# Optimization experiments

Measured on AMD Instinct MI355X. Metric: run time of the kernel, lower is better.

Reference implementation:

```python
import jax, jax.numpy as jnp
from jax import lax
import numpy as np

B, CIN, COUT, H, W = 32, 64, 64, 128, 128
KH = KW = 1
STRIDE = (1, 1)
PADDING = ((0, 0), (0, 0))


def setup_inputs() -> dict:
    key = jax.random.key(0)
    k1, k2, k3, k4 = jax.random.split(key, 4)
    x_quant = jax.random.randint(k1, (B, CIN, H, W), 0, 256, dtype=jnp.int32)  # uint8 values
    weight_int8 = jax.random.randint(k2, (COUT, CIN, KH, KW), -127, 128, dtype=jnp.int32)
    weight_scale = jax.random.uniform(k3, (COUT, 1, 1, 1), dtype=jnp.float32, minval=0.001, maxval=0.02)
    weight_zero_point = jnp.zeros((COUT, 1, 1, 1), dtype=jnp.int32)
    bias_fp32 = jax.random.normal(k4, (COUT,), dtype=jnp.float32) * 0.1
    return {
        "x_quant": x_quant,
        "input_scale": jnp.float32(0.02),
        "input_zero_point": jnp.int32(128),
        "weight_int8": weight_int8,
        "weight_scale": weight_scale,
        "weight_zero_point": weight_zero_point,
        "bias_fp32": bias_fp32,
        "output_scale": jnp.float32(0.05),
        "output_zero_point": jnp.int32(128),
    }


def reference(x_quant, input_scale, input_zero_point, weight_int8, weight_scale,
              weight_zero_point, bias_fp32, output_scale, output_zero_point):
    # dequant (zero-point subtract) in fp32
    x = x_quant.astype(jnp.float32) - input_zero_point.astype(jnp.float32)          # [B,Cin,H,W]
    w = weight_int8.astype(jnp.float32) - weight_zero_point.astype(jnp.float32)     # [O,I,kh,kw]
    conv = lax.conv_general_dilated(
        x, w, window_strides=STRIDE, padding=PADDING,
        dimension_numbers=("NCHW", "OIHW", "NCHW"))                                 # [B,O,H',W']
    # requantize: per-out-channel scale + bias, round, clamp to uint8 range
    requant_scale = (input_scale * weight_scale / output_scale).reshape(1, COUT, 1, 1)
    bias_term = (bias_fp32 / output_scale).reshape(1, COUT, 1, 1)
    final_float = conv * requant_scale + bias_term
    requant = jnp.round(final_float) + output_zero_point.astype(jnp.float32)
    out_q = jnp.clip(requant, 0.0, 255.0).astype(jnp.uint8)
    return out_q
```

## Files before the change

### kernel.cpp

```cpp
#include <hip/hip_runtime.h>

#define CIN   64
#define COUT  64
#define HW    16384
#define NPIX  (32 * HW)
#define HALF  (NPIX / 2)

__global__ void prep_kernel(const int* __restrict__ w,
                            const float* __restrict__ wscale,
                            const int* __restrict__ wzp,
                            const float* __restrict__ bias,
                            const float* __restrict__ is_p,
                            const int* __restrict__ izp_p,
                            const float* __restrict__ os_p,
                            const int* __restrict__ ozp_p,
                            int* __restrict__ wp,
                            float4* __restrict__ params) {
    int o = threadIdx.x;
    if (o >= COUT) return;
    int zp = wzp[o];
    int sum = 0;
    #pragma unroll
    for (int k = 0; k < 16; ++k) {
        int c0 = w[o * CIN + 4 * k + 0] - zp;
        int c1 = w[o * CIN + 4 * k + 1] - zp;
        int c2 = w[o * CIN + 4 * k + 2] - zp;
        int c3 = w[o * CIN + 4 * k + 3] - zp;
        sum += c0 + c1 + c2 + c3;
        wp[o * 16 + k] = (c0 & 0xff) | ((c1 & 0xff) << 8) |
                         ((c2 & 0xff) << 16) | ((c3 & 0xff) << 24);
    }
    float4 pr;
    pr.x = is_p[0] * wscale[o] / os_p[0];
    pr.y = bias[o] / os_p[0] + (float)ozp_p[0];
    pr.z = 0.0f;
    pr.w = __int_as_float((128 - izp_p[0]) * sum);
    params[o] = pr;
}

__device__ __forceinline__ int pack4(int v0, int v1, int v2, int v3) {
    return (v0 | (v1 << 8) | (v2 << 16) | (v3 << 24)) ^ 0x80808080;
}

__global__ __launch_bounds__(128) void conv_kernel(
    const int* __restrict__ x,
    const int* __restrict__ wp_g,
    const float4* __restrict__ params_g,
    int* __restrict__ out) {

    const int tid = threadIdx.x;
    const int t0  = blockIdx.x * 128 + tid;

    #pragma unroll
    for (int half = 0; half < 2; ++half) {
        int t = t0 + half * HALF;
        int b = t >> 14;
        int p = t & (HW - 1);

        const int* xb = x + b * (CIN * HW) + p;

        int pk[16];
        #pragma unroll
        for (int cg = 0; cg < 16; ++cg) {
            int v0 = xb[(4 * cg + 0) * HW];
            int v1 = xb[(4 * cg + 1) * HW];
            int v2 = xb[(4 * cg + 2) * HW];
            int v3 = xb[(4 * cg + 3) * HW];
            pk[cg] = pack4(v0, v1, v2, v3);
        }

        int* ob = out + b * (COUT * HW) + p;

        #pragma unroll 8
        for (int o = 0; o < COUT; ++o) {
            const int4* wv = (const int4*)(wp_g + o * 16);
            int4 w0 = wv[0], w1 = wv[1], w2 = wv[2], w3 = wv[3];
            float4 pr = params_g[o];
            int acc = __float_as_int(pr.w);

            acc = __builtin_amdgcn_sdot4(pk[0],  w0.x, acc, false);
            acc = __builtin_amdgcn_sdot4(pk[1],  w0.y, acc, false);
            acc = __builtin_amdgcn_sdot4(pk[2],  w0.z, acc, false);
            acc = __builtin_amdgcn_sdot4(pk[3],  w0.w, acc, false);
            acc = __builtin_amdgcn_sdot4(pk[4],  w1.x, acc, false);
            acc = __builtin_amdgcn_sdot4(pk[5],  w1.y, acc, false);
            acc = __builtin_amdgcn_sdot4(pk[6],  w1.z, acc, false);
            acc = __builtin_amdgcn_sdot4(pk[7],  w1.w, acc, false);
            acc = __builtin_amdgcn_sdot4(pk[8],  w2.x, acc, false);
            acc = __builtin_amdgcn_sdot4(pk[9],  w2.y, acc, false);
            acc = __builtin_amdgcn_sdot4(pk[10], w2.z, acc, false);
            acc = __builtin_amdgcn_sdot4(pk[11], w2.w, acc, false);
            acc = __builtin_amdgcn_sdot4(pk[12], w3.x, acc, false);
            acc = __builtin_amdgcn_sdot4(pk[13], w3.y, acc, false);
            acc = __builtin_amdgcn_sdot4(pk[14], w3.z, acc, false);
            acc = __builtin_amdgcn_sdot4(pk[15], w3.w, acc, false);

            float f = fmaf((float)acc, pr.x, pr.y);
            f = rintf(f);
            f = fminf(fmaxf(f, 0.0f), 255.0f);
            __builtin_nontemporal_store((int)f, ob + o * HW);
        }
    }
}

extern "C" void kernel_launch(void* const* d_in, const int* in_sizes, int n_in,
                              void* d_out, int out_size, void* d_ws, size_t ws_size,
                              hipStream_t stream) {
    const int*   x      = (const int*)d_in[0];
    const float* is_p   = (const float*)d_in[1];
    const int*   izp_p  = (const int*)d_in[2];
    const int*   w      = (const int*)d_in[3];
    const float* wscale = (const float*)d_in[4];
    const int*   wzp    = (const int*)d_in[5];
    const float* bias   = (const float*)d_in[6];
    const float* os_p   = (const float*)d_in[7];
    const int*   ozp_p  = (const int*)d_in[8];

    int* out = (int*)d_out;

    int*    wp     = (int*)d_ws;
    float4* params = (float4*)((char*)d_ws + 4096);

    prep_kernel<<<1, 64, 0, stream>>>(w, wscale, wzp, bias, is_p, izp_p, os_p,
                                      ozp_p, wp, params);

    conv_kernel<<<2048, 128, 0, stream>>>(x, wp, params, out);
}
```

Before: 258.1 us.

## Prefetch second pixel's input channels while computing first pixel's outputs

Each thread handles two pixels. The loads for the second pixel's 64 input channels are now issued in chunks of 16, interleaved with the output computation and stores for the first pixel, so memory latency overlaps with sdot4 work. The aim is to hide load latency in a memory-bound kernel, at the cost of more live registers (16 raw values plus two packed arrays), which could lower occupancy.

```diff
diff --git a/kernel.cpp b/kernel.cpp
--- a/kernel.cpp
+++ b/kernel.cpp
@@ -42,65 +42,84 @@
     return (v0 | (v1 << 8) | (v2 << 16) | (v3 << 24)) ^ 0x80808080;
 }
 
+__device__ __forceinline__ void out_chunk(int o0,
+                                          const int* __restrict__ wp_g,
+                                          const float4* __restrict__ params_g,
+                                          const int pk[16],
+                                          int* __restrict__ ob) {
+    #pragma unroll
+    for (int i = 0; i < 16; ++i) {
+        int o = o0 + i;
+        const int4* wv = (const int4*)(wp_g + o * 16);
+        int4 w0 = wv[0], w1 = wv[1], w2 = wv[2], w3 = wv[3];
+        float4 pr = params_g[o];
+        int acc = __float_as_int(pr.w);
+
+        acc = __builtin_amdgcn_sdot4(pk[0],  w0.x, acc, false);
+        acc = __builtin_amdgcn_sdot4(pk[1],  w0.y, acc, false);
+        acc = __builtin_amdgcn_sdot4(pk[2],  w0.z, acc, false);
+        acc = __builtin_amdgcn_sdot4(pk[3],  w0.w, acc, false);
+        acc = __builtin_amdgcn_sdot4(pk[4],  w1.x, acc, false);
+        acc = __builtin_amdgcn_sdot4(pk[5],  w1.y, acc, false);
+        acc = __builtin_amdgcn_sdot4(pk[6],  w1.z, acc, false);
+        acc = __builtin_amdgcn_sdot4(pk[7],  w1.w, acc, false);
+        acc = __builtin_amdgcn_sdot4(pk[8],  w2.x, acc, false);
+        acc = __builtin_amdgcn_sdot4(pk[9],  w2.y, acc, false);
+        acc = __builtin_amdgcn_sdot4(pk[10], w2.z, acc, false);
+        acc = __builtin_amdgcn_sdot4(pk[11], w2.w, acc, false);
+        acc = __builtin_amdgcn_sdot4(pk[12], w3.x, acc, false);
+        acc = __builtin_amdgcn_sdot4(pk[13], w3.y, acc, false);
+        acc = __builtin_amdgcn_sdot4(pk[14], w3.z, acc, false);
+        acc = __builtin_amdgcn_sdot4(pk[15], w3.w, acc, false);
+
+        float f = fmaf((float)acc, pr.x, pr.y);
+        f = rintf(f);
+        f = fminf(fmaxf(f, 0.0f), 255.0f);
+        __builtin_nontemporal_store((int)f, ob + o * HW);
+    }
+}
+
 __global__ __launch_bounds__(128) void conv_kernel(
     const int* __restrict__ x,
     const int* __restrict__ wp_g,
     const float4* __restrict__ params_g,
     int* __restrict__ out) {
 
-    const int tid = threadIdx.x;
-    const int t0  = blockIdx.x * 128 + tid;
+    const int t = blockIdx.x * 128 + threadIdx.x;
+    const int bA = t >> 14, pA = t & (HW - 1);
+    const int tB = t + HALF;
+    const int bB = tB >> 14, pB = tB & (HW - 1);
+
+    const int* xA = x + bA * (CIN * HW) + pA;
+    const int* xB = x + bB * (CIN * HW) + pB;
+    int* obA = out + bA * (COUT * HW) + pA;
+    int* obB = out + bB * (COUT * HW) + pB;
+
+    int pkA[16];
+    #pragma unroll
+    for (int cg = 0; cg < 16; ++cg)
+        pkA[cg] = pack4(xA[(4 * cg + 0) * HW], xA[(4 * cg + 1) * HW],
+                        xA[(4 * cg + 2) * HW], xA[(4 * cg + 3) * HW]);
+
+    int pkB[16];
+    #pragma unroll
+    for (int c = 0; c < 4; ++c) {
+        int raw[16];
+        #pragma unroll
+        for (int j = 0; j < 16; ++j)
+            raw[j] = xB[(16 * c + j) * HW];
+
+        out_chunk(16 * c, wp_g, params_g, pkA, obA);
+
+        #pragma unroll
+        for (int g = 0; g < 4; ++g)
+            pkB[4 * c + g] = pack4(raw[4 * g + 0], raw[4 * g + 1],
+                                   raw[4 * g + 2], raw[4 * g + 3]);
+    }
 
     #pragma unroll
-    for (int half = 0; half < 2; ++half) {
-        int t = t0 + half * HALF;
-        int b = t >> 14;
-        int p = t & (HW - 1);
-
-        const int* xb = x + b * (CIN * HW) + p;
-
-        int pk[16];
-        #pragma unroll
-        for (int cg = 0; cg < 16; ++cg) {
-            int v0 = xb[(4 * cg + 0) * HW];
-            int v1 = xb[(4 * cg + 1) * HW];
-            int v2 = xb[(4 * cg + 2) * HW];
-            int v3 = xb[(4 * cg + 3) * HW];
-            pk[cg] = pack4(v0, v1, v2, v3);
-        }
-
-        int* ob = out + b * (COUT * HW) + p;
-
-        #pragma unroll 8
-        for (int o = 0; o < COUT; ++o) {
-            const int4* wv = (const int4*)(wp_g + o * 16);
-            int4 w0 = wv[0], w1 = wv[1], w2 = wv[2], w3 = wv[3];
-            float4 pr = params_g[o];
-            int acc = __float_as_int(pr.w);
-
-            acc = __builtin_amdgcn_sdot4(pk[0],  w0.x, acc, false);
-            acc = __builtin_amdgcn_sdot4(pk[1],  w0.y, acc, false);
-            acc = __builtin_amdgcn_sdot4(pk[2],  w0.z, acc, false);
-            acc = __builtin_amdgcn_sdot4(pk[3],  w0.w, acc, false);
-            acc = __builtin_amdgcn_sdot4(pk[4],  w1.x, acc, false);
-            acc = __builtin_amdgcn_sdot4(pk[5],  w1.y, acc, false);
-            acc = __builtin_amdgcn_sdot4(pk[6],  w1.z, acc, false);
-            acc = __builtin_amdgcn_sdot4(pk[7],  w1.w, acc, false);
-            acc = __builtin_amdgcn_sdot4(pk[8],  w2.x, acc, false);
-            acc = __builtin_amdgcn_sdot4(pk[9],  w2.y, acc, false);
-            acc = __builtin_amdgcn_sdot4(pk[10], w2.z, acc, false);
-            acc = __builtin_amdgcn_sdot4(pk[11], w2.w, acc, false);
-            acc = __builtin_amdgcn_sdot4(pk[12], w3.x, acc, false);
-            acc = __builtin_amdgcn_sdot4(pk[13], w3.y, acc, false);
-            acc = __builtin_amdgcn_sdot4(pk[14], w3.z, acc, false);
-            acc = __builtin_amdgcn_sdot4(pk[15], w3.w, acc, false);
-
-            float f = fmaf((float)acc, pr.x, pr.y);
-            f = rintf(f);
-            f = fminf(fmaxf(f, 0.0f), 255.0f);
-            __builtin_nontemporal_store((int)f, ob + o * HW);
-        }
-    }
+    for (int c = 0; c < 4; ++c)
+        out_chunk(16 * c, wp_g, params_g, pkB, obB);
 }
 
 extern "C" void kernel_launch(void* const* d_in, const int* in_sizes, int n_in,
```

After: 283.6 us. 9.9% more time.

## Map lanes to output channels with readlane broadcast and LDS-transposed stores

Applied to the files above, without the earlier changes.

Each lane now owns one output channel and keeps its packed weights in registers. Per pixel, the packed activations are broadcast across the wave with readlane, and the results are transposed through shared memory so the global stores stay coalesced. This removes the repeated per-output-channel weight loads from global memory and the second pass over pixels per thread. In exchange it adds readlane instructions (scalar-register traffic) and an LDS round trip, and it serialises pixels within a wave. Correctness depends on the readlane and LDS reads within a single wave being ordered without a barrier.

```diff
diff --git a/kernel.cpp b/kernel.cpp
--- a/kernel.cpp
+++ b/kernel.cpp
@@ -4,7 +4,9 @@
 #define COUT  64
 #define HW    16384
 #define NPIX  (32 * HW)
-#define HALF  (NPIX / 2)
+
+#define TILE  64
+#define TPAD  17
 
 __global__ void prep_kernel(const int* __restrict__ w,
                             const float* __restrict__ wscale,
@@ -42,63 +44,75 @@
     return (v0 | (v1 << 8) | (v2 << 16) | (v3 << 24)) ^ 0x80808080;
 }
 
-__global__ __launch_bounds__(128) void conv_kernel(
+__global__ __launch_bounds__(256, 4) void conv_kernel(
     const int* __restrict__ x,
     const int* __restrict__ wp_g,
     const float4* __restrict__ params_g,
     int* __restrict__ out) {
 
-    const int tid = threadIdx.x;
-    const int t0  = blockIdx.x * 128 + tid;
+    __shared__ int s_t[4][COUT * TPAD];
 
+    const int tid  = threadIdx.x;
+    const int lane = tid & 63;
+    const int wv   = tid >> 6;
+
+    const int4* wvp = (const int4*)(wp_g + lane * 16);
+    int4 w0 = wvp[0], w1 = wvp[1], w2 = wvp[2], w3 = wvp[3];
+    float4 pr = params_g[lane];
+    const int accbase = __float_as_int(pr.w);
+
+    const int tile = blockIdx.x * 4 + wv;
+    const int t0   = tile * TILE;
+    const int b    = t0 >> 14;
+    const int p0   = t0 & (HW - 1);
+
+    const int* xb = x + b * (CIN * HW) + p0 + lane;
+    int pk[16];
     #pragma unroll
-    for (int half = 0; half < 2; ++half) {
-        int t = t0 + half * HALF;
-        int b = t >> 14;
-        int p = t & (HW - 1);
+    for (int cg = 0; cg < 16; ++cg) {
+        int v0 = xb[(4 * cg + 0) * HW];
+        int v1 = xb[(4 * cg + 1) * HW];
+        int v2 = xb[(4 * cg + 2) * HW];
+        int v3 = xb[(4 * cg + 3) * HW];
+        pk[cg] = pack4(v0, v1, v2, v3);
+    }
 
-        const int* xb = x + b * (CIN * HW) + p;
+    int* ob = out + b * (COUT * HW) + p0;
+    int* lds = s_t[wv];
 
-        int pk[16];
+    const int q    = lane >> 4;
+    const int px15 = lane & 15;
+
+    for (int s = 0; s < 4; ++s) {
         #pragma unroll
-        for (int cg = 0; cg < 16; ++cg) {
-            int v0 = xb[(4 * cg + 0) * HW];
-            int v1 = xb[(4 * cg + 1) * HW];
-            int v2 = xb[(4 * cg + 2) * HW];
-            int v3 = xb[(4 * cg + 3) * HW];
-            pk[cg] = pack4(v0, v1, v2, v3);
-        }
+        for (int pp = 0; pp < 16; ++pp) {
+            const int p = s * 16 + pp;
 
-        int* ob = out + b * (COUT * HW) + p;
-
-        #pragma unroll 8
-        for (int o = 0; o < COUT; ++o) {
-            const int4* wv = (const int4*)(wp_g + o * 16);
-            int4 w0 = wv[0], w1 = wv[1], w2 = wv[2], w3 = wv[3];
-            float4 pr = params_g[o];
-            int acc = __float_as_int(pr.w);
-
-            acc = __builtin_amdgcn_sdot4(pk[0],  w0.x, acc, false);
-            acc = __builtin_amdgcn_sdot4(pk[1],  w0.y, acc, false);
-            acc = __builtin_amdgcn_sdot4(pk[2],  w0.z, acc, false);
-            acc = __builtin_amdgcn_sdot4(pk[3],  w0.w, acc, false);
-            acc = __builtin_amdgcn_sdot4(pk[4],  w1.x, acc, false);
-            acc = __builtin_amdgcn_sdot4(pk[5],  w1.y, acc, false);
-            acc = __builtin_amdgcn_sdot4(pk[6],  w1.z, acc, false);
-            acc = __builtin_amdgcn_sdot4(pk[7],  w1.w, acc, false);
-            acc = __builtin_amdgcn_sdot4(pk[8],  w2.x, acc, false);
-            acc = __builtin_amdgcn_sdot4(pk[9],  w2.y, acc, false);
-            acc = __builtin_amdgcn_sdot4(pk[10], w2.z, acc, false);
-            acc = __builtin_amdgcn_sdot4(pk[11], w2.w, acc, false);
-            acc = __builtin_amdgcn_sdot4(pk[12], w3.x, acc, false);
-            acc = __builtin_amdgcn_sdot4(pk[13], w3.y, acc, false);
-            acc = __builtin_amdgcn_sdot4(pk[14], w3.z, acc, false);
-            acc = __builtin_amdgcn_sdot4(pk[15], w3.w, acc, false);
+            int acc = accbase;
+            #pragma unroll
+            for (int j = 0; j < 4; ++j) {
+                int b0 = __builtin_amdgcn_readlane(pk[4 * j + 0], p);
+                int b1 = __builtin_amdgcn_readlane(pk[4 * j + 1], p);
+                int b2 = __builtin_amdgcn_readlane(pk[4 * j + 2], p);
+                int b3 = __builtin_amdgcn_readlane(pk[4 * j + 3], p);
+                const int4& wj = (j == 0) ? w0 : (j == 1) ? w1 : (j == 2) ? w2 : w3;
+                acc = __builtin_amdgcn_sdot4(b0, wj.x, acc, false);
+                acc = __builtin_amdgcn_sdot4(b1, wj.y, acc, false);
+                acc = __builtin_amdgcn_sdot4(b2, wj.z, acc, false);
+                acc = __builtin_amdgcn_sdot4(b3, wj.w, acc, false);
+            }
 
             float f = fmaf((float)acc, pr.x, pr.y);
             f = rintf(f);
             f = fminf(fmaxf(f, 0.0f), 255.0f);
-            __builtin_nontemporal_store((int)f, ob + o * HW);
+            lds[lane * TPAD + pp] = (int)f;
+        }
+
+        #pragma unroll
+        for (int i = 0; i < 16; ++i) {
+            int oo = q + 4 * i;
+            int v = lds[oo * TPAD + px15];
+            __builtin_nontemporal_store(v, ob + oo * HW + s * 16 + px15);
         }
     }
 }
@@ -124,5 +138,5 @@
     prep_kernel<<<1, 64, 0, stream>>>(w, wscale, wzp, bias, is_p, izp_p, os_p,
                                       ozp_p, wp, params);
 
-    conv_kernel<<<2048, 128, 0, stream>>>(x, wp, params, out);
+    conv_kernel<<<2048, 256, 0, stream>>>(x, wp, params, out);
 }
```

After: 270.1 us. 4.6% more time.
